# Kernel tuning notes

Measured on AMD Instinct MI355X. Metric: run time of the kernel, lower is better.

Reference implementation:

```python
import jax, jax.numpy as jnp
import numpy as np

B, N = 2, 4096
IN_CH, OUT_CH = 64, 64
L_MAX, NR = 3, 4
KERNEL_RADIUS = 0.5
PATCH = 64  # hardcoded in torch topk(-dist, 64)


def setup_inputs() -> dict:
    key = jax.random.key(0)
    k1, k2, k3 = jax.random.split(key, 3)
    xyz = jax.random.normal(k1, (B, N, 3), dtype=jnp.float32)
    signal = jax.random.normal(k2, (B, N, IN_CH), dtype=jnp.float32)
    # xavier_uniform on (out, in, nr, l_max+1): receptive = nr*(l_max+1)
    recept = NR * (L_MAX + 1)
    bound = float(np.sqrt(6.0 / (IN_CH * recept + OUT_CH * recept)))
    weight = jax.random.uniform(k3, (OUT_CH, IN_CH, NR, L_MAX + 1), dtype=jnp.float32,
                                minval=-bound, maxval=bound)
    biases = jnp.zeros((OUT_CH,), dtype=jnp.float32)
    return {"xyz": xyz, "signal": signal, "weight": weight, "biases": biases}


def _sph(X):
    # X: [B,N,P,3] l2-normalized patch directions -> [B,N,P,(L_MAX+1)^2]
    x, y, z = X[..., 0], X[..., 1], X[..., 2]
    x2, y2, z2 = x * x, y * y, z * z
    Ys = []
    Ys.append(jnp.full_like(x, 0.5 * np.sqrt(1.0 / np.pi)))           # Y00
    s3 = np.sqrt(3.0 / np.pi) / 2.0
    Ys += [s3 * y, s3 * z, -s3 * x]                                    # l=1
    s15h = np.sqrt(15.0 / np.pi) / 2.0
    s15q = np.sqrt(15.0 / np.pi) / 4.0
    s5q = np.sqrt(5.0 / np.pi) / 4.0
    Ys += [s15h * x * y, s15h * y * z, s5q * (2.0 * z2 - x2 - y2),
           -s15h * z * x, s15q * (x2 - y2)]                            # l=2
    c33 = np.sqrt(35.0 / (2.0 * np.pi)) / 4.0
    c32 = np.sqrt(105.0 / np.pi) / 2.0
    c31 = np.sqrt(21.0 / (2.0 * np.pi)) / 4.0
    c30 = np.sqrt(7.0 / np.pi) / 4.0
    c32b = np.sqrt(105.0 / np.pi) / 4.0
    Ys += [c33 * (3.0 * x2 * y - y * y2),
           c32 * x * y * z,
           c31 * (4.0 * y * z2 - x2 * y - y * y2),
           c30 * (2.0 * z * z2 - 3.0 * x2 * z - 3.0 * y2 * z),
           -c31 * (4.0 * z2 * x - x * x2 - x * y2),
           c32b * (x2 * z - y2 * z),
           -c33 * (x * x2 - 3.0 * x * y2)]                             # l=3
    return jnp.stack(Ys, axis=-1)


def reference(xyz, signal, weight, biases):
    # pairwise squared distances via matmul (costly_cdist)
    r2 = jnp.sum(xyz * xyz, axis=2)                                    # [B,N]
    sqd = r2[:, :, None] - 2.0 * jnp.einsum('bnd,bmd->bnm', xyz, xyz) + r2[:, None, :]
    neg_vals, idx = jax.lax.top_k(-sqd, PATCH)                         # KNN
    sq_patches_dist = -neg_vals                                        # [B,N,P]
    gather = jax.vmap(lambda pts, i: pts[i])                           # per-batch fancy gather
    patches = gather(xyz, idx) - xyz[:, :, None, :]                    # [B,N,P,3]
    # F.normalize(p=2, dim=-1, eps=0.01): x / max(||x||, eps)
    nrm = jnp.linalg.norm(patches, axis=-1, keepdims=True)
    Y = _sph(patches / jnp.maximum(nrm, 0.01))                         # [B,N,P,K2]
    dist = jnp.sqrt(jnp.maximum(sq_patches_dist, 1e-4))                # [B,N,P]
    r_grid = jnp.linspace(0.0, KERNEL_RADIUS, NR, dtype=jnp.float32)   # [NR]
    sigma = KERNEL_RADIUS / (NR - 1)
    rad = jnp.exp(-jnp.square(dist[..., None] - r_grid) / (2.0 * sigma ** 2))  # [B,N,P,NR]
    yk = Y[:, :, :, None, :] * rad[..., None]                          # [B,N,P,NR,K2]
    y_w = jnp.sum(yk[:, :, :, 0, 0], axis=2)[:, :, None, None, None]   # [B,N,1,1,1]
    conv_kernel = yk / (y_w + 1e-6)
    sig_patches = gather(signal, idx)                                  # [B,N,P,C]
    y = jnp.einsum('bvprn,bvpc->bvcrn', conv_kernel, sig_patches)
    y = y * y
    bands = [jnp.sum(y[..., l * l:(l + 1) * (l + 1)], axis=-1) for l in range(L_MAX + 1)]
    y = jnp.stack(bands, axis=-1)                                      # [B,N,C,NR,L+1]
    y = jnp.sqrt(jnp.maximum(y, 1e-4))
    out = jnp.einsum('ijrn,bvjrn->bvi', weight, y) + biases
    return out
```

## Files before the change

kernel.cpp:

```cpp
#include <hip/hip_runtime.h>
#include <hip/hip_bf16.h>
#include <math.h>

#define NB 2
#define NPTS 4096
#define CH 64
#define PATCH 64

typedef __attribute__((ext_vector_type(8))) short s16x8;
typedef __attribute__((ext_vector_type(4))) short s16x4;
typedef __attribute__((ext_vector_type(4))) float f32x4;
typedef __attribute__((ext_vector_type(4))) unsigned u32x4;

static __device__ __forceinline__ short f2bf(float f) {
    union { __hip_bfloat16 h; short s; } u;
    u.h = __float2bfloat16(f);
    return u.s;
}

__global__ __launch_bounds__(256) void wprep_kernel(const float* __restrict__ W,
                                                    short* __restrict__ Wfrag) {
    const int gid = blockIdx.x * 256 + threadIdx.x;
    const int mt = gid >> 11;
    const int st = (gid >> 6) & 31;
    const int l  = gid & 63;
    const int i  = mt * 16 + (l & 15);
    const int k0 = st * 32 + (l >> 4) * 8;
    const f32x4 a = *(const f32x4*)&W[i * 1024 + k0];
    const f32x4 c = *(const f32x4*)&W[i * 1024 + k0 + 4];
    s16x8 v;
    v[0] = f2bf(a[0]); v[1] = f2bf(a[1]); v[2] = f2bf(a[2]); v[3] = f2bf(a[3]);
    v[4] = f2bf(c[0]); v[5] = f2bf(c[1]); v[6] = f2bf(c[2]); v[7] = f2bf(c[3]);
    *(s16x8*)&Wfrag[gid * 8] = v;
}

__global__ __launch_bounds__(256, 8) void knn_kernel(const float* __restrict__ xyz,
                                                     int* __restrict__ knn_idx) {
    const int pt   = blockIdx.x;
    const int b    = pt >> 12;
    const int q    = pt & (NPTS - 1);
    const int tid  = threadIdx.x;
    const int wv   = tid >> 6;
    const int lane = tid & 63;

    __shared__ __align__(16) unsigned hist[4096];
    __shared__ unsigned wsum[4];
    __shared__ unsigned sh_H;
    __shared__ int sh_need;
    __shared__ int cnt_less, cnt_tie;

    const float* xb = xyz + (size_t)b * NPTS * 3;
    const float qx = xb[q * 3 + 0];
    const float qy = xb[q * 3 + 1];
    const float qz = xb[q * 3 + 2];

#pragma unroll
    for (int u = 0; u < 4; ++u)
        ((u32x4*)hist)[u * 256 + tid] = (u32x4){0u, 0u, 0u, 0u};
    if (tid == 0) { cnt_less = 0; cnt_tie = 0; }
    __syncthreads();

    for (int m = tid; m < NPTS; m += 256) {
        const float dx = xb[m * 3 + 0] - qx;
        const float dy = xb[m * 3 + 1] - qy;
        const float dz = xb[m * 3 + 2] - qz;
        const float sq = fmaf(dx, dx, fmaf(dy, dy, dz * dz));
        atomicAdd(&hist[__float_as_uint(sq) >> 19], 1u);
    }
    __syncthreads();

    unsigned tsum = 0;
#pragma unroll
    for (int u = 0; u < 4; ++u) {
        const u32x4 h4 = ((const u32x4*)hist)[tid * 4 + u];
        tsum += h4[0] + h4[1] + h4[2] + h4[3];
    }
    unsigned run = tsum;
#pragma unroll
    for (int off = 1; off < 64; off <<= 1) {
        const unsigned v = __shfl_up(run, off);
        if (lane >= off) run += v;
    }
    if (lane == 63) wsum[wv] = run;
    __syncthreads();
    unsigned wbase = 0;
    for (int w2 = 0; w2 < wv; ++w2) wbase += wsum[w2];
    const unsigned incl = wbase + run;
    const unsigned excl = incl - tsum;
    if ((int)excl < PATCH && PATCH <= (int)incl) {
        int nrem = PATCH - (int)excl;
        for (int u = 0; u < 16; ++u) {
            const unsigned cb = hist[tid * 16 + u];
            if (nrem <= (int)cb) { sh_H = (unsigned)(tid * 16 + u); sh_need = nrem; break; }
            nrem -= (int)cb;
        }
    }
    __syncthreads();

    const unsigned H = sh_H;
    const int need  = sh_need;
    const int nless = PATCH - need;
    unsigned* ckey = hist;
    unsigned* cidx = hist + 2048;

    for (int m = tid; m < NPTS; m += 256) {
        const float dx = xb[m * 3 + 0] - qx;
        const float dy = xb[m * 3 + 1] - qy;
        const float dz = xb[m * 3 + 2] - qz;
        const float sq = fmaf(dx, dx, fmaf(dy, dy, dz * dz));
        const unsigned key = __float_as_uint(sq);
        const unsigned hk = key >> 19;
        if (hk < H) {
            const int pos = atomicAdd(&cnt_less, 1);
            knn_idx[pt * PATCH + pos] = m;
        } else if (hk == H) {
            const int pos = atomicAdd(&cnt_tie, 1);
            if (pos < 2048) { ckey[pos] = key; cidx[pos] = m; }
        }
    }
    __syncthreads();

    const int nc = min(cnt_tie, 2048);
    for (int i = tid; i < nc; i += 256) {
        const unsigned ki = ckey[i];
        int rank = 0;
        for (int j = 0; j < nc; ++j) {
            const unsigned kj = ckey[j];
            rank += (kj < ki || (kj == ki && j < i)) ? 1 : 0;
        }
        if (rank < need) knn_idx[pt * PATCH + nless + rank] = cidx[i];
    }
}

__global__ __launch_bounds__(256, 4) void conv_kernel(const float* __restrict__ xyz,
                                                      const float* __restrict__ signal,
                                                      const short* __restrict__ Wfrag,
                                                      const float* __restrict__ biases,
                                                      const int* __restrict__ knn_idx,
                                                      float* __restrict__ out) {
    const int tid  = threadIdx.x;
    const int wv   = tid >> 6;
    const int lane = tid & 63;
    const int ln15 = lane & 15;
    const int kq   = lane >> 4;

    __shared__ __align__(16) short cks_bf[4096];
    __shared__ __align__(16) short ckF[4096];
    __shared__ __align__(16) short sigF[4096];
    __shared__ __align__(16) short zb[4 * 1032];
    __shared__ int   sIdx[PATCH];
    __shared__ float sh_inv;

    for (int it = 0; it < 4; ++it) {
        const int pt = blockIdx.x * 4 + it;
        const int b  = pt >> 12;
        const int q  = pt & (NPTS - 1);

        if (tid < PATCH) sIdx[tid] = knn_idx[pt * PATCH + tid];
        __syncthreads();

        if (wv == 0) {
            const int p   = lane;
            const int idx = sIdx[p];
            const float cx = xyz[(b * NPTS + q) * 3 + 0];
            const float cy = xyz[(b * NPTS + q) * 3 + 1];
            const float cz = xyz[(b * NPTS + q) * 3 + 2];
            const float dx = xyz[(b * NPTS + idx) * 3 + 0] - cx;
            const float dy = xyz[(b * NPTS + idx) * 3 + 1] - cy;
            const float dz = xyz[(b * NPTS + idx) * 3 + 2] - cz;
            const float nrm2 = dx * dx + dy * dy + dz * dz;
            const float inv_n = 1.0f / fmaxf(sqrtf(nrm2), 0.01f);
            const float x = dx * inv_n, y = dy * inv_n, z = dz * inv_n;
            const float x2 = x * x, y2 = y * y, zz = z * z;

            float Y[16];
            Y[0] = 0.28209479177387814f;
            const float s3 = 0.4886025119029199f;
            Y[1] = s3 * y;  Y[2] = s3 * z;  Y[3] = -s3 * x;
            const float s15h = 1.0925484305920792f;
            const float s15q = 0.5462742152960396f;
            const float s5q  = 0.31539156525252005f;
            Y[4] = s15h * x * y;
            Y[5] = s15h * y * z;
            Y[6] = s5q * (2.0f * zz - x2 - y2);
            Y[7] = -s15h * z * x;
            Y[8] = s15q * (x2 - y2);
            const float c33  = 0.5900435899266435f;
            const float c32  = 2.8906114426405543f;
            const float c31  = 0.4570457994644658f;
            const float c30  = 0.3731763325901154f;
            const float c32b = 1.4453057213202771f;
            Y[9]  = c33 * (3.0f * x2 * y - y * y2);
            Y[10] = c32 * x * y * z;
            Y[11] = c31 * (4.0f * y * zz - x2 * y - y * y2);
            Y[12] = c30 * (2.0f * z * zz - 3.0f * x2 * z - 3.0f * y2 * z);
            Y[13] = -c31 * (4.0f * zz * x - x * x2 - x * y2);
            Y[14] = c32b * (x2 * z - y2 * z);
            Y[15] = -c33 * (x * x2 - 3.0f * x * y2);

            const float dist = sqrtf(fmaxf(nrm2, 1e-4f));
            const float d1 = dist - 0.16666667f;
            const float d2 = dist - 0.33333334f;
            const float d3 = dist - 0.5f;
            float rad[4];
            rad[0] = expf(-dist * dist * 18.0f);
            rad[1] = expf(-d1 * d1 * 18.0f);
            rad[2] = expf(-d2 * d2 * 18.0f);
            rad[3] = expf(-d3 * d3 * 18.0f);

            const int pm = p & 15;
#pragma unroll
            for (int chunk = 0; chunk < 16; ++chunk) {
                const int r  = chunk >> 2;
                const int kb = (chunk & 3) * 4;
                s16x4 v;
                v[0] = f2bf(Y[kb + 0] * rad[r]);
                v[1] = f2bf(Y[kb + 1] * rad[r]);
                v[2] = f2bf(Y[kb + 2] * rad[r]);
                v[3] = f2bf(Y[kb + 3] * rad[r]);
                *(s16x4*)&cks_bf[p * 64 + ((chunk ^ pm) << 2)] = v;
            }
            float v = 0.28209479177387814f * rad[0];
#pragma unroll
            for (int off = 32; off > 0; off >>= 1) v += __shfl_down(v, off);
            if (p == 0) sh_inv = 1.0f / (v + 1e-6f);
        } else {
            const int r0 = (wv - 1) * 3;
            const int rn = (wv == 3) ? 2 : 3;
            for (int rr = 0; rr < rn; ++rr) {
                const int rd = r0 + rr;
                const int ct = rd >> 1, s = rd & 1;
                const int c  = ct * 16 + ln15;
                const int pb = s * 32 + kq * 8;
                s16x8 sv;
#pragma unroll
                for (int j = 0; j < 8; ++j) {
                    const float f = signal[(size_t)(b * NPTS + sIdx[pb + j]) * CH + c];
                    sv[j] = f2bf(f);
                }
                *(s16x8*)&sigF[(ct * 2 + s) * 512 + lane * 8] = sv;
            }
        }
        __syncthreads();

#pragma unroll
        for (int ff = 0; ff < 2; ++ff) {
            const int f  = wv + ff * 4;
            const int mt = f >> 1, s = f & 1;
            const int rk = mt * 16 + ln15;
            const int rsw = rk >> 2, rlo = rk & 3;
            const int pb = s * 32 + kq * 8;
            s16x8 av;
#pragma unroll
            for (int j = 0; j < 8; ++j) {
                const int p = pb + j;
                av[j] = cks_bf[p * 64 + ((rsw ^ (p & 15)) << 2) + rlo];
            }
            *(s16x8*)&ckF[f * 512 + lane * 8] = av;
        }
        __syncthreads();

        const s16x8 bf0 = *(const s16x8*)&sigF[(wv * 2 + 0) * 512 + lane * 8];
        const s16x8 bf1 = *(const s16x8*)&sigF[(wv * 2 + 1) * 512 + lane * 8];
        f32x4 acc0 = {0.f, 0.f, 0.f, 0.f}, acc1 = acc0, acc2 = acc0, acc3 = acc0;
        {
            s16x8 a;
            a = *(const s16x8*)&ckF[0 * 512 + lane * 8];
            acc0 = __builtin_amdgcn_mfma_f32_16x16x32_bf16(a, bf0, acc0, 0, 0, 0);
            a = *(const s16x8*)&ckF[1 * 512 + lane * 8];
            acc0 = __builtin_amdgcn_mfma_f32_16x16x32_bf16(a, bf1, acc0, 0, 0, 0);
            a = *(const s16x8*)&ckF[2 * 512 + lane * 8];
            acc1 = __builtin_amdgcn_mfma_f32_16x16x32_bf16(a, bf0, acc1, 0, 0, 0);
            a = *(const s16x8*)&ckF[3 * 512 + lane * 8];
            acc1 = __builtin_amdgcn_mfma_f32_16x16x32_bf16(a, bf1, acc1, 0, 0, 0);
            a = *(const s16x8*)&ckF[4 * 512 + lane * 8];
            acc2 = __builtin_amdgcn_mfma_f32_16x16x32_bf16(a, bf0, acc2, 0, 0, 0);
            a = *(const s16x8*)&ckF[5 * 512 + lane * 8];
            acc2 = __builtin_amdgcn_mfma_f32_16x16x32_bf16(a, bf1, acc2, 0, 0, 0);
            a = *(const s16x8*)&ckF[6 * 512 + lane * 8];
            acc3 = __builtin_amdgcn_mfma_f32_16x16x32_bf16(a, bf0, acc3, 0, 0, 0);
            a = *(const s16x8*)&ckF[7 * 512 + lane * 8];
            acc3 = __builtin_amdgcn_mfma_f32_16x16x32_bf16(a, bf1, acc3, 0, 0, 0);
        }

        const float inv = sh_inv;
        const int qq = kq;
        float rb[4][4];
#pragma unroll
        for (int mt = 0; mt < 4; ++mt) {
            f32x4 av = (mt == 0) ? acc0 : (mt == 1) ? acc1 : (mt == 2) ? acc2 : acc3;
            const float y0 = av[0] * inv, y1 = av[1] * inv;
            const float y2 = av[2] * inv, y3 = av[3] * inv;
            const float sA = y0 * y0;
            const float sB = y1 * y1 + y2 * y2 + y3 * y3;
            const float sAll = sA + sB;
            float b0 = (qq == 0) ? sA : 0.0f;
            float b1 = (qq == 0) ? sB : 0.0f;
            float b2 = (qq == 1) ? sAll : ((qq == 2) ? sA : 0.0f);
            float b3 = (qq == 3) ? sAll : ((qq == 2) ? sB : 0.0f);
            b0 += __shfl_xor(b0, 16); b0 += __shfl_xor(b0, 32);
            b1 += __shfl_xor(b1, 16); b1 += __shfl_xor(b1, 32);
            b2 += __shfl_xor(b2, 16); b2 += __shfl_xor(b2, 32);
            b3 += __shfl_xor(b3, 16); b3 += __shfl_xor(b3, 32);
            rb[mt][0] = b0; rb[mt][1] = b1; rb[mt][2] = b2; rb[mt][3] = b3;
        }
        float s0 = rb[0][0], s1 = rb[0][1], s2 = rb[0][2], s3 = rb[0][3];
#pragma unroll
        for (int mt = 1; mt < 4; ++mt) {
            s0 = (qq == mt) ? rb[mt][0] : s0;
            s1 = (qq == mt) ? rb[mt][1] : s1;
            s2 = (qq == mt) ? rb[mt][2] : s2;
            s3 = (qq == mt) ? rb[mt][3] : s3;
        }
        s16x4 zv;
        zv[0] = f2bf(sqrtf(fmaxf(s0, 1e-4f)));
        zv[1] = f2bf(sqrtf(fmaxf(s1, 1e-4f)));
        zv[2] = f2bf(sqrtf(fmaxf(s2, 1e-4f)));
        zv[3] = f2bf(sqrtf(fmaxf(s3, 1e-4f)));
        const int c = wv * 16 + ln15;
        *(s16x4*)&zb[it * 1032 + c * 16 + qq * 4] = zv;
    }
    __syncthreads();

    const int mt5 = wv;
    const int g   = ln15 & 3;
    f32x4 acc5 = {0.f, 0.f, 0.f, 0.f};
#pragma unroll 4
    for (int st = 0; st < 32; ++st) {
        const s16x8 a  = *(const s16x8*)&Wfrag[((mt5 * 32 + st) * 64 + lane) * 8];
        const s16x8 zf = *(const s16x8*)&zb[g * 1032 + st * 32 + kq * 8];
        acc5 = __builtin_amdgcn_mfma_f32_16x16x32_bf16(a, zf, acc5, 0, 0, 0);
    }
    if (ln15 < 4) {
        const int i0 = mt5 * 16 + kq * 4;
        const int orow = (blockIdx.x * 4 + g) * CH;
#pragma unroll
        for (int rg = 0; rg < 4; ++rg)
            out[orow + i0 + rg] = acc5[rg] + biases[i0 + rg];
    }
}

extern "C" void kernel_launch(void* const* d_in, const int* in_sizes, int n_in,
                              void* d_out, int out_size, void* d_ws, size_t ws_size,
                              hipStream_t stream) {
    const float* xyz    = (const float*)d_in[0];
    const float* signal = (const float*)d_in[1];
    const float* weight = (const float*)d_in[2];
    const float* biases = (const float*)d_in[3];
    float* out = (float*)d_out;

    int*   knn_idx = (int*)d_ws;
    short* Wfrag   = (short*)((char*)d_ws + (size_t)NB * NPTS * PATCH * sizeof(int));

    wprep_kernel<<<32, 256, 0, stream>>>(weight, Wfrag);
    knn_kernel<<<NB * NPTS, 256, 0, stream>>>(xyz, knn_idx);
    conv_kernel<<<(NB * NPTS) / 4, 256, 0, stream>>>(xyz, signal, Wfrag, biases,
                                                     knn_idx, out);
}
```

Before: 92.33 us.

## Pad xyz to float4 and cache histogram bins in LDS for kNN

A combined prep kernel converts the weights and also repacks xyz into padded float4, so each point is fetched with one vector load instead of three scalar loads. The kNN kernel stores each candidate's 13-bit bin in shared memory during the histogram pass. The second pass then reads bins from LDS instead of reloading and recomputing every distance, and only recomputes exact keys for points in the tie bin. The extra 8KB of LDS per block forces the occupancy hint down from 8 to 6 blocks, which may reduce latency hiding.

Result: slower. 94.98 us (+2.9%).

```diff
diff --git a/kernel.cpp b/kernel.cpp
--- a/kernel.cpp
+++ b/kernel.cpp
@@ -18,23 +18,37 @@
     return u.s;
 }
 
-__global__ __launch_bounds__(256) void wprep_kernel(const float* __restrict__ W,
-                                                    short* __restrict__ Wfrag) {
-    const int gid = blockIdx.x * 256 + threadIdx.x;
-    const int mt = gid >> 11;
-    const int st = (gid >> 6) & 31;
-    const int l  = gid & 63;
-    const int i  = mt * 16 + (l & 15);
-    const int k0 = st * 32 + (l >> 4) * 8;
-    const f32x4 a = *(const f32x4*)&W[i * 1024 + k0];
-    const f32x4 c = *(const f32x4*)&W[i * 1024 + k0 + 4];
-    s16x8 v;
-    v[0] = f2bf(a[0]); v[1] = f2bf(a[1]); v[2] = f2bf(a[2]); v[3] = f2bf(a[3]);
-    v[4] = f2bf(c[0]); v[5] = f2bf(c[1]); v[6] = f2bf(c[2]); v[7] = f2bf(c[3]);
-    *(s16x8*)&Wfrag[gid * 8] = v;
-}
-
-__global__ __launch_bounds__(256, 8) void knn_kernel(const float* __restrict__ xyz,
+__global__ __launch_bounds__(256) void prep_kernel(const float* __restrict__ W,
+                                                   short* __restrict__ Wfrag,
+                                                   const float* __restrict__ xyz,
+                                                   float4* __restrict__ xyz4) {
+    const int bid = blockIdx.x;
+    const int tid = threadIdx.x;
+    if (bid < 32) {
+        const int gid = bid * 256 + tid;
+        const int mt = gid >> 11;
+        const int st = (gid >> 6) & 31;
+        const int l  = gid & 63;
+        const int i  = mt * 16 + (l & 15);
+        const int k0 = st * 32 + (l >> 4) * 8;
+        const f32x4 a = *(const f32x4*)&W[i * 1024 + k0];
+        const f32x4 c = *(const f32x4*)&W[i * 1024 + k0 + 4];
+        s16x8 v;
+        v[0] = f2bf(a[0]); v[1] = f2bf(a[1]); v[2] = f2bf(a[2]); v[3] = f2bf(a[3]);
+        v[4] = f2bf(c[0]); v[5] = f2bf(c[1]); v[6] = f2bf(c[2]); v[7] = f2bf(c[3]);
+        *(s16x8*)&Wfrag[gid * 8] = v;
+    } else {
+        const int idx = (bid - 32) * 256 + tid;
+        float4 v;
+        v.x = xyz[idx * 3 + 0];
+        v.y = xyz[idx * 3 + 1];
+        v.z = xyz[idx * 3 + 2];
+        v.w = 0.0f;
+        xyz4[idx] = v;
+    }
+}
+
+__global__ __launch_bounds__(256, 6) void knn_kernel(const float4* __restrict__ xyz4,
                                                      int* __restrict__ knn_idx) {
     const int pt   = blockIdx.x;
     const int b    = pt >> 12;
@@ -44,15 +58,14 @@
     const int lane = tid & 63;
 
     __shared__ __align__(16) unsigned hist[4096];
+    __shared__ __align__(16) unsigned short sbin[4096];
     __shared__ unsigned wsum[4];
     __shared__ unsigned sh_H;
     __shared__ int sh_need;
     __shared__ int cnt_less, cnt_tie;
 
-    const float* xb = xyz + (size_t)b * NPTS * 3;
-    const float qx = xb[q * 3 + 0];
-    const float qy = xb[q * 3 + 1];
-    const float qz = xb[q * 3 + 2];
+    const float4* xb = xyz4 + (size_t)b * NPTS;
+    const float4 qp = xb[q];
 
 #pragma unroll
     for (int u = 0; u < 4; ++u)
@@ -60,12 +73,17 @@
     if (tid == 0) { cnt_less = 0; cnt_tie = 0; }
     __syncthreads();
 
-    for (int m = tid; m < NPTS; m += 256) {
-        const float dx = xb[m * 3 + 0] - qx;
-        const float dy = xb[m * 3 + 1] - qy;
-        const float dz = xb[m * 3 + 2] - qz;
+#pragma unroll 4
+    for (int i = 0; i < 16; ++i) {
+        const int m = i * 256 + tid;
+        const float4 p = xb[m];
+        const float dx = p.x - qp.x;
+        const float dy = p.y - qp.y;
+        const float dz = p.z - qp.z;
         const float sq = fmaf(dx, dx, fmaf(dy, dy, dz * dz));
-        atomicAdd(&hist[__float_as_uint(sq) >> 19], 1u);
+        const unsigned hk = __float_as_uint(sq) >> 19;
+        sbin[i * 256 + tid] = (unsigned short)hk;
+        atomicAdd(&hist[hk], 1u);
     }
     __syncthreads();
 
@@ -100,22 +118,28 @@
     const unsigned H = sh_H;
     const int need  = sh_need;
     const int nless = PATCH - need;
+    int* optr = knn_idx + (size_t)pt * PATCH;
     unsigned* ckey = hist;
     unsigned* cidx = hist + 2048;
 
-    for (int m = tid; m < NPTS; m += 256) {
-        const float dx = xb[m * 3 + 0] - qx;
-        const float dy = xb[m * 3 + 1] - qy;
-        const float dz = xb[m * 3 + 2] - qz;
-        const float sq = fmaf(dx, dx, fmaf(dy, dy, dz * dz));
-        const unsigned key = __float_as_uint(sq);
-        const unsigned hk = key >> 19;
+#pragma unroll 4
+    for (int i = 0; i < 16; ++i) {
+        const int m = i * 256 + tid;
+        const unsigned hk = sbin[i * 256 + tid];
         if (hk < H) {
             const int pos = atomicAdd(&cnt_less, 1);
-            knn_idx[pt * PATCH + pos] = m;
+            optr[pos] = m;
         } else if (hk == H) {
             const int pos = atomicAdd(&cnt_tie, 1);
-            if (pos < 2048) { ckey[pos] = key; cidx[pos] = m; }
+            if (pos < 2048) {
+                const float4 p = xb[m];
+                const float dx = p.x - qp.x;
+                const float dy = p.y - qp.y;
+                const float dz = p.z - qp.z;
+                const float sq = fmaf(dx, dx, fmaf(dy, dy, dz * dz));
+                ckey[pos] = __float_as_uint(sq);
+                cidx[pos] = m;
+            }
         }
     }
     __syncthreads();
@@ -128,11 +152,11 @@
             const unsigned kj = ckey[j];
             rank += (kj < ki || (kj == ki && j < i)) ? 1 : 0;
         }
-        if (rank < need) knn_idx[pt * PATCH + nless + rank] = cidx[i];
-    }
-}
-
-__global__ __launch_bounds__(256, 4) void conv_kernel(const float* __restrict__ xyz,
+        if (rank < need) optr[nless + rank] = cidx[i];
+    }
+}
+
+__global__ __launch_bounds__(256, 4) void conv_kernel(const float4* __restrict__ xyz4,
                                                       const float* __restrict__ signal,
                                                       const short* __restrict__ Wfrag,
                                                       const float* __restrict__ biases,
@@ -156,18 +180,17 @@
         const int b  = pt >> 12;
         const int q  = pt & (NPTS - 1);
 
-        if (tid < PATCH) sIdx[tid] = knn_idx[pt * PATCH + tid];
+        if (tid < PATCH) sIdx[tid] = knn_idx[(size_t)pt * PATCH + tid];
         __syncthreads();
 
         if (wv == 0) {
             const int p   = lane;
             const int idx = sIdx[p];
-            const float cx = xyz[(b * NPTS + q) * 3 + 0];
-            const float cy = xyz[(b * NPTS + q) * 3 + 1];
-            const float cz = xyz[(b * NPTS + q) * 3 + 2];
-            const float dx = xyz[(b * NPTS + idx) * 3 + 0] - cx;
-            const float dy = xyz[(b * NPTS + idx) * 3 + 1] - cy;
-            const float dz = xyz[(b * NPTS + idx) * 3 + 2] - cz;
+            const float4 cp = xyz4[(size_t)b * NPTS + q];
+            const float4 np = xyz4[(size_t)b * NPTS + idx];
+            const float dx = np.x - cp.x;
+            const float dy = np.y - cp.y;
+            const float dz = np.z - cp.z;
             const float nrm2 = dx * dx + dy * dy + dz * dz;
             const float inv_n = 1.0f / fmaxf(sqrtf(nrm2), 0.01f);
             const float x = dx * inv_n, y = dy * inv_n, z = dz * inv_n;
@@ -349,11 +372,13 @@
     const float* biases = (const float*)d_in[3];
     float* out = (float*)d_out;
 
-    int*   knn_idx = (int*)d_ws;
-    short* Wfrag   = (short*)((char*)d_ws + (size_t)NB * NPTS * PATCH * sizeof(int));
-
-    wprep_kernel<<<32, 256, 0, stream>>>(weight, Wfrag);
-    knn_kernel<<<NB * NPTS, 256, 0, stream>>>(xyz, knn_idx);
-    conv_kernel<<<(NB * NPTS) / 4, 256, 0, stream>>>(xyz, signal, Wfrag, biases,
+    char* ws = (char*)d_ws;
+    int*    knn_idx = (int*)ws;
+    short*  Wfrag   = (short*)(ws + (size_t)NB * NPTS * PATCH * sizeof(int));
+    float4* xyz4    = (float4*)(ws + (size_t)NB * NPTS * PATCH * sizeof(int) + 131072);
+
+    prep_kernel<<<64, 256, 0, stream>>>(weight, Wfrag, xyz, xyz4);
+    knn_kernel<<<NB * NPTS, 256, 0, stream>>>(xyz4, knn_idx);
+    conv_kernel<<<(NB * NPTS) / 4, 256, 0, stream>>>(xyz4, signal, Wfrag, biases,
                                                      knn_idx, out);
 }
```
